# Optimization experiments

Measured on AMD Instinct MI355X. Metric: run time of the kernel, lower is better.

Reference implementation:

```python
import jax, jax.numpy as jnp
import numpy as np
from jax import lax

STRIDES = (8, 16, 32, 64, 128)
LEVEL_HW = ((100, 128), (50, 64), (25, 32), (13, 16), (7, 8))
NUM_CLASSES = 80
PRE_NMS_THRESH = 0.05
PRE_NMS_TOPK = 1000
NMS_THRESH = 0.6
MAX_DET = 100
CLS_OFFSET = 1.0e4  # > max image coordinate, separates classes for joint NMS


def setup_inputs() -> dict:
    key = jax.random.key(0)
    B = 16
    ks = jax.random.split(key, 3 * len(LEVEL_HW))
    inp = {}
    i = 0
    for lvl, (h, w) in enumerate(LEVEL_HW):
        # shift logits down so sigmoid scores are mostly below the 0.05 candidate
        # threshold (realistic detection sparsity)
        inp[f"logits_p{lvl + 3}"] = jax.random.normal(ks[i], (B, NUM_CLASSES, h, w), jnp.float32) - 4.0; i += 1
        inp[f"bbox_p{lvl + 3}"] = jax.random.uniform(ks[i], (B, 4, h, w), jnp.float32, minval=0.0, maxval=64.0); i += 1
        inp[f"ctr_p{lvl + 3}"] = jax.random.normal(ks[i], (B, 1, h, w), jnp.float32); i += 1
    inp["im_info"] = jnp.tile(jnp.array([[800.0, 1024.0]], jnp.float32), (B, 1))
    return inp


def _locations(h, w, stride):
    # FCOSLocation: center of each stride cell -> [HW, 2] as (x, y)
    sx = jnp.arange(w, dtype=jnp.float32) * stride + stride // 2
    sy = jnp.arange(h, dtype=jnp.float32) * stride + stride // 2
    yy, xx = jnp.meshgrid(sy, sx, indexing="ij")
    return jnp.stack([xx.reshape(-1), yy.reshape(-1)], axis=-1)


def _nms_single(boxes, scores, classes):
    # boxes [K,4], scores [K] (descending), classes [K] int
    off = classes.astype(jnp.float32)[:, None] * CLS_OFFSET
    nb = boxes + off  # class-offset trick -> per-class NMS in one pass
    areas = jnp.maximum(nb[:, 2] - nb[:, 0], 0.0) * jnp.maximum(nb[:, 3] - nb[:, 1], 0.0)

    def body(sc, _):
        i = jnp.argmax(sc)
        s = sc[i]
        bi = nb[i]
        xx1 = jnp.maximum(bi[0], nb[:, 0])
        yy1 = jnp.maximum(bi[1], nb[:, 1])
        xx2 = jnp.minimum(bi[2], nb[:, 2])
        yy2 = jnp.minimum(bi[3], nb[:, 3])
        inter = jnp.maximum(xx2 - xx1, 0.0) * jnp.maximum(yy2 - yy1, 0.0)
        iou = inter / (areas[i] + areas - inter + 1e-9)
        sc2 = jnp.where(iou >= NMS_THRESH, -jnp.inf, sc).at[i].set(-jnp.inf)
        return sc2, (i, s > 0.0)

    _, (idxs, valid) = lax.scan(body, scores, None, length=MAX_DET)
    det = jnp.concatenate(
        [boxes[idxs], scores[idxs][:, None], classes[idxs].astype(jnp.float32)[:, None]],
        axis=-1,
    )  # [MAX_DET, 6] = x1,y1,x2,y2,score,class
    return jnp.where(valid[:, None], det, 0.0)


def _forward(logits_p3, bbox_p3, ctr_p3, logits_p4, bbox_p4, ctr_p4,
             logits_p5, bbox_p5, ctr_p5, logits_p6, bbox_p6, ctr_p6,
             logits_p7, bbox_p7, ctr_p7, im_info):
    levels = [(logits_p3, bbox_p3, ctr_p3), (logits_p4, bbox_p4, ctr_p4),
              (logits_p5, bbox_p5, ctr_p5), (logits_p6, bbox_p6, ctr_p6),
              (logits_p7, bbox_p7, ctr_p7)]
    scores_l, boxes_l = [], []
    for (lg, rg, ct), stride in zip(levels, STRIDES):
        B, C, H, W = lg.shape
        cls = jax.nn.sigmoid(lg).transpose(0, 2, 3, 1).reshape(B, H * W, C)
        cen = jax.nn.sigmoid(ct).transpose(0, 2, 3, 1).reshape(B, H * W, 1)
        # candidate threshold on raw class prob, then modulate by centerness
        comb = jnp.where(cls > PRE_NMS_THRESH, cls * cen, 0.0)
        locs = _locations(H, W, stride)  # [HW, 2]
        reg = rg.transpose(0, 2, 3, 1).reshape(B, H * W, 4)  # (l, t, r, b)
        bx = jnp.stack([locs[None, :, 0] - reg[..., 0],
                        locs[None, :, 1] - reg[..., 1],
                        locs[None, :, 0] + reg[..., 2],
                        locs[None, :, 1] + reg[..., 3]], axis=-1)
        scores_l.append(comb)
        boxes_l.append(bx)
    scores = jnp.concatenate(scores_l, axis=1)  # [B, N, C]
    boxes = jnp.concatenate(boxes_l, axis=1)    # [B, N, 4]
    B, N, C = scores.shape
    vals, idx = lax.top_k(scores.reshape(B, N * C), PRE_NMS_TOPK)  # [B, K]
    loc = idx // C
    cls_id = idx % C
    cand = jnp.take_along_axis(boxes, loc[..., None], axis=1)  # [B, K, 4]
    h = im_info[:, 0:1]
    w = im_info[:, 1:2]
    x1 = jnp.clip(cand[..., 0], 0.0, w - 1.0)
    y1 = jnp.clip(cand[..., 1], 0.0, h - 1.0)
    x2 = jnp.clip(cand[..., 2], 0.0, w - 1.0)
    y2 = jnp.clip(cand[..., 3], 0.0, h - 1.0)
    cand = jnp.stack([x1, y1, x2, y2], axis=-1)
    sc = jnp.where(vals > 0.0, jnp.sqrt(jnp.maximum(vals, 0.0) + 1e-12), 0.0)
    return jax.vmap(_nms_single)(cand, sc, cls_id)  # [B, MAX_DET, 6]


def reference(logits_p3, bbox_p3, ctr_p3, logits_p4, bbox_p4, ctr_p4,
              logits_p5, bbox_p5, ctr_p5, logits_p6, bbox_p6, ctr_p6,
              logits_p7, bbox_p7, ctr_p7, im_info):
    return _forward(logits_p3, bbox_p3, ctr_p3, logits_p4, bbox_p4, ctr_p4,
                    logits_p5, bbox_p5, ctr_p5, logits_p6, bbox_p6, ctr_p6,
                    logits_p7, bbox_p7, ctr_p7, im_info)
```

## Files before the change

kernel.cpp:

```cpp
#include <hip/hip_runtime.h>
#include <math.h>

#pragma clang fp contract(off)

#define NB 16
#define NC 80
#define NTOT 17064
#define TOPK 1000
#define NBINS 8192
#define CAP 4096
#define MAXDET 100
#define NREP 2
#define CNTSTRIDE 64
#define CHUNK 128

struct Ptrs {
    const float* lg[5];
    const float* bb[5];
    const float* ct[5];
};

__device__ __forceinline__ void level_of(int n, int& l, int& hw, int& W,
                                         int& stride, int& half, int& HW) {
    if (n < 12800)      { l = 0; hw = n;         W = 128; stride = 8;   half = 4;  HW = 12800; }
    else if (n < 16000) { l = 1; hw = n - 12800; W = 64;  stride = 16;  half = 8;  HW = 3200;  }
    else if (n < 16800) { l = 2; hw = n - 16000; W = 32;  stride = 32;  half = 16; HW = 800;   }
    else if (n < 17008) { l = 3; hw = n - 16800; W = 16;  stride = 64;  half = 32; HW = 208;   }
    else                { l = 4; hw = n - 17008; W = 8;   stride = 128; half = 64; HW = 56;    }
}

__device__ __forceinline__ float fast_sig(float x) {
    float e = __expf(-x);
    return __builtin_amdgcn_rcpf(1.0f + e);
}

template<int HW4, int NF4>
__device__ __forceinline__ void hist_level(const float* lgb, const float* ctb,
                                           int tid, int bx, int gx, unsigned* lh) {
    for (int i0 = bx * 256; i0 < NF4; i0 += gx * 256) {
        int i = i0 + tid;
        if (i < NF4) {
            int c   = i / HW4;
            int hwf = i - c * HW4;
            float4 v  = *(const float4*)(lgb + c * (HW4 * 4) + hwf * 4);
            if (v.x > -2.95f || v.y > -2.95f || v.z > -2.95f || v.w > -2.95f) {
                float4 cv = *(const float4*)(ctb + hwf * 4);
                float xs[4] = {v.x, v.y, v.z, v.w};
                float cs[4] = {cv.x, cv.y, cv.z, cv.w};
#pragma unroll
                for (int j = 0; j < 4; ++j) {
                    float x = xs[j];
                    if (x > -2.95f) {
                        float cls = fast_sig(x);
                        if (cls > 0.04999f) {
                            bool in = true;
                            if (cls < 0.05001f) {
                                float ex = 1.0f / (1.0f + expf(-x));
                                in = ex > 0.05f;
                            }
                            if (in) {
                                float cen = fast_sig(cs[j]);
                                float comb = cls * cen;
                                unsigned bits = __float_as_uint(comb);
                                bits = (bits > 32u) ? bits - 32u : 0u;
                                atomicAdd(&lh[bits >> 19], 1u);
                            }
                        }
                    }
                }
            }
        }
    }
}

__global__ void __launch_bounds__(256) k_histA(Ptrs p, unsigned* hist) {
    __shared__ unsigned lh[NBINS];
    int b = blockIdx.y, tid = threadIdx.x, bx = blockIdx.x, gx = gridDim.x;
    for (int i = tid; i < NBINS; i += 256) lh[i] = 0;
    __syncthreads();

    hist_level<3200, 256000>(p.lg[0] + (size_t)b * NC * 12800, p.ct[0] + (size_t)b * 12800, tid, bx, gx, lh);
    hist_level< 800,  64000>(p.lg[1] + (size_t)b * NC * 3200,  p.ct[1] + (size_t)b * 3200,  tid, bx, gx, lh);
    hist_level< 200,  16000>(p.lg[2] + (size_t)b * NC * 800,   p.ct[2] + (size_t)b * 800,   tid, bx, gx, lh);
    hist_level<  52,   4160>(p.lg[3] + (size_t)b * NC * 208,   p.ct[3] + (size_t)b * 208,   tid, bx, gx, lh);
    hist_level<  14,   1120>(p.lg[4] + (size_t)b * NC * 56,    p.ct[4] + (size_t)b * 56,    tid, bx, gx, lh);

    __syncthreads();
    unsigned* h = hist + ((size_t)(bx & (NREP - 1)) * NB + b) * NBINS;
    for (int i = tid; i < NBINS; i += 256) {
        unsigned v = lh[i];
        if (v) atomicAdd(&h[i], v);
    }
}

__global__ void __launch_bounds__(256) k_thresh(const unsigned* hist, unsigned* T) {
    __shared__ unsigned hl[NBINS];
    __shared__ unsigned wtot[4];
    __shared__ int Tf;
    int b = blockIdx.x, tid = threadIdx.x, lane = tid & 63, wv = tid >> 6;
    if (tid == 0) Tf = 0;
    for (int i = tid; i < NBINS; i += 256) {
        unsigned s = 0;
        for (int r = 0; r < NREP; ++r)
            s += hist[((size_t)r * NB + b) * NBINS + i];
        hl[i] = s;
    }
    __syncthreads();
    int base = tid * 32;
    unsigned mysum = 0;
#pragma unroll
    for (int i = 0; i < 32; ++i) mysum += hl[base + i];
    unsigned incl = mysum;
#pragma unroll
    for (int off = 1; off < 64; off <<= 1) {
        unsigned v = __shfl_down(incl, off);
        if (lane + off < 64) incl += v;
    }
    if (lane == 0) wtot[wv] = incl;
    __syncthreads();
    unsigned above = 0;
    for (int w = wv + 1; w < 4; ++w) above += wtot[w];
    unsigned sufincl = incl + above;
    unsigned excl = sufincl - mysum;
    if (excl < TOPK && sufincl >= TOPK) {
        unsigned running = excl;
        for (int bin = base + 31; bin >= base; --bin) {
            running += hl[bin];
            if (running >= TOPK) { Tf = bin; break; }
        }
    }
    __syncthreads();
    if (tid == 0) T[b] = (unsigned)Tf;
}

template<int HW4, int NF4, int LVOFF>
__device__ __forceinline__ void compact_level(const float* lgb, const float* ctb,
        int tid, int lane, int bx, int gx, unsigned Tb, float xpre,
        unsigned* cntb, unsigned long long* selb, unsigned long long ltmask) {
    for (int i0 = bx * 256; i0 < NF4; i0 += gx * 256) {
        int i = i0 + tid;
        bool f0 = false, f1 = false, f2 = false, f3 = false;
        unsigned long long k0 = 0, k1 = 0, k2 = 0, k3 = 0;
        if (i < NF4) {
            int c   = i / HW4;
            int hwf = i - c * HW4;
            float4 v = *(const float4*)(lgb + c * (HW4 * 4) + hwf * 4);
            if (v.x > xpre || v.y > xpre || v.z > xpre || v.w > xpre) {
                float4 cv = *(const float4*)(ctb + hwf * 4);
                int nbase = LVOFF + hwf * 4;
#define DO_J(J, X, CT, F, K)                                                  \
                if ((X) > xpre) {                                             \
                    float cls = 1.0f / (1.0f + expf(-(X)));                   \
                    if (cls > 0.05f) {                                        \
                        float cen = 1.0f / (1.0f + expf(-(CT)));              \
                        float comb = cls * cen;                               \
                        unsigned bits = __float_as_uint(comb);                \
                        if ((bits >> 19) >= Tb) {                             \
                            unsigned idx = (unsigned)((nbase + (J)) * NC + c);\
                            K = ((unsigned long long)bits << 32) |            \
                                (0xFFFFFFFFu - idx);                          \
                            F = true;                                         \
                        }                                                     \
                    }                                                         \
                }
                DO_J(0, v.x, cv.x, f0, k0)
                DO_J(1, v.y, cv.y, f1, k1)
                DO_J(2, v.z, cv.z, f2, k2)
                DO_J(3, v.w, cv.w, f3, k3)
#undef DO_J
            }
        }
        unsigned long long m0 = __ballot(f0), m1 = __ballot(f1);
        unsigned long long m2 = __ballot(f2), m3 = __ballot(f3);
        if ((m0 | m1 | m2 | m3) == 0ULL) continue;
        unsigned t0 = (unsigned)__popcll(m0), t1 = (unsigned)__popcll(m1);
        unsigned t2 = (unsigned)__popcll(m2), t3 = (unsigned)__popcll(m3);
        unsigned total = t0 + t1 + t2 + t3;
        int basep = 0;
        if (lane == 0) basep = (int)atomicAdd(cntb, total);
        basep = __shfl(basep, 0);
        if (f0) { int pos = basep + (int)__popcll(m0 & ltmask);                       if (pos < CAP) selb[pos] = k0; }
        if (f1) { int pos = basep + (int)t0 + (int)__popcll(m1 & ltmask);             if (pos < CAP) selb[pos] = k1; }
        if (f2) { int pos = basep + (int)(t0 + t1) + (int)__popcll(m2 & ltmask);      if (pos < CAP) selb[pos] = k2; }
        if (f3) { int pos = basep + (int)(t0 + t1 + t2) + (int)__popcll(m3 & ltmask); if (pos < CAP) selb[pos] = k3; }
    }
}

__global__ void __launch_bounds__(256) k_compactB(Ptrs p, const unsigned* T,
                                                  unsigned* cnt2, unsigned long long* sel) {
    int b = blockIdx.y, tid = threadIdx.x, lane = tid & 63;
    int bx = blockIdx.x, gx = gridDim.x;
    unsigned Tb = T[b];
    float mthr = __uint_as_float(Tb << 19);
    float xpre = -2.95f;
    if (mthr > 1e-37f && mthr < 1.0f) {
        float lm = logf(mthr / (1.0f - mthr)) - 0.01f;
        if (lm > xpre) xpre = lm;
    }
    unsigned long long ltmask = (1ULL << lane) - 1ULL;
    unsigned* cntb = cnt2 + (size_t)b * CNTSTRIDE;
    unsigned long long* selb = sel + (size_t)b * CAP;
    compact_level<3200, 256000,     0>(p.lg[0] + (size_t)b * NC * 12800, p.ct[0] + (size_t)b * 12800, tid, lane, bx, gx, Tb, xpre, cntb, selb, ltmask);
    compact_level< 800,  64000, 12800>(p.lg[1] + (size_t)b * NC * 3200,  p.ct[1] + (size_t)b * 3200,  tid, lane, bx, gx, Tb, xpre, cntb, selb, ltmask);
    compact_level< 200,  16000, 16000>(p.lg[2] + (size_t)b * NC * 800,   p.ct[2] + (size_t)b * 800,   tid, lane, bx, gx, Tb, xpre, cntb, selb, ltmask);
    compact_level<  52,   4160, 16800>(p.lg[3] + (size_t)b * NC * 208,   p.ct[3] + (size_t)b * 208,   tid, lane, bx, gx, Tb, xpre, cntb, selb, ltmask);
    compact_level<  14,   1120, 17008>(p.lg[4] + (size_t)b * NC * 56,    p.ct[4] + (size_t)b * 56,    tid, lane, bx, gx, Tb, xpre, cntb, selb, ltmask);
}

__global__ void __launch_bounds__(256) k_rankdec(Ptrs p, const unsigned* cnt,
                                                 const unsigned long long* sel,
                                                 const float* im_info, float* cand) {
    __shared__ __align__(16) unsigned long long keys[CAP];
    int b = blockIdx.y, tid = threadIdx.x;
    unsigned M = cnt[(size_t)b * CNTSTRIDE];
    if (M > CAP) M = CAP;
    int s0 = blockIdx.x * 256;
    if (s0 >= (int)M) return;
    int Mpad = (int)((M + 1u) & ~1u);
    for (int i = tid; i < Mpad; i += 256)
        keys[i] = (i < (int)M) ? sel[(size_t)b * CAP + i] : 0ULL;
    __syncthreads();

    int s = s0 + tid;
    if (s >= (int)M) return;
    unsigned long long k = keys[s];
    int rank = 0;
    for (int j = 0; j < Mpad; j += 2) {
        ulonglong2 kk = *(const ulonglong2*)&keys[j];
        rank += (kk.x > k) ? 1 : 0;
        rank += (kk.y > k) ? 1 : 0;
    }
    if (rank >= TOPK) return;

    float Him = im_info[b * 2 + 0], Wim = im_info[b * 2 + 1];
    float xmax = Wim - 1.0f, ymax = Him - 1.0f;
    unsigned sb = (unsigned)(k >> 32);
    unsigned idx = 0xFFFFFFFFu - (unsigned)(k & 0xFFFFFFFFu);
    float val = __uint_as_float(sb);
    int n = idx / NC, c = idx - n * NC;
    int l, hw, W, stride, half, HW;
    level_of(n, l, hw, W, stride, half, HW);
    int wx = hw % W, hy = hw / W;
    float locx = (float)(wx * stride + half);
    float locy = (float)(hy * stride + half);
    const float* bb = p.bb[l] + (size_t)b * 4 * HW + hw;
    float r0 = bb[0], r1 = bb[(size_t)HW], r2 = bb[(size_t)2 * HW], r3 = bb[(size_t)3 * HW];
    float x1 = locx - r0, y1 = locy - r1, x2 = locx + r2, y2 = locy + r3;
    x1 = fminf(fmaxf(x1, 0.f), xmax);
    y1 = fminf(fmaxf(y1, 0.f), ymax);
    x2 = fminf(fmaxf(x2, 0.f), xmax);
    y2 = fminf(fmaxf(y2, 0.f), ymax);
    float scv = sqrtf(val + 1e-12f);
    float off = (float)c * 10000.0f;
    float a0 = x1 + off, a1 = y1 + off, a2 = x2 + off, a3 = y2 + off;
    float area = fmaxf(a2 - a0, 0.f) * fmaxf(a3 - a1, 0.f);
    float* dst = cand + ((size_t)b * TOPK + rank) * 12;
    *(float4*)(dst + 0) = make_float4(x1, y1, x2, y2);
    *(float4*)(dst + 4) = make_float4(a0, a1, a2, a3);
    *(float4*)(dst + 8) = make_float4(area, scv, (float)c, 0.f);
}

__global__ void __launch_bounds__(64) k_nms(const unsigned* cnt, const float* cand,
                                            float* out) {
    __shared__ float4 s_ob[CHUNK], s_nb[CHUNK], s_ms[CHUNK];
    int b = blockIdx.x, lane = threadIdx.x;
    unsigned M = cnt[(size_t)b * CNTSTRIDE];
    if (M > CAP) M = CAP;
    int ncand = (int)M < TOPK ? (int)M : TOPK;
    const float* src = cand + (size_t)b * TOPK * 12;
    float* ob = out + (size_t)b * MAXDET * 6;

    int na = 0;
    float4 a0b = make_float4(0.f, 0.f, 0.f, 0.f);
    float4 a1b = make_float4(0.f, 0.f, 0.f, 0.f);
    float a0a = 0.f, a1a = 0.f;

    for (int base = 0; base < ncand && na < MAXDET; base += CHUNK) {
        int cn = ncand - base; if (cn > CHUNK) cn = CHUNK;
        for (int cidx = lane; cidx < cn; cidx += 64) {
            const float* s = src + (size_t)(base + cidx) * 12;
            s_ob[cidx] = *(const float4*)(s + 0);
            s_nb[cidx] = *(const float4*)(s + 4);
            s_ms[cidx] = *(const float4*)(s + 8);
        }
        __syncthreads();
        for (int r = 0; r < cn && na < MAXDET; ++r) {
            float4 cb = s_nb[r];
            float ca = s_ms[r].x;
            bool sup = false;
            if (lane < na) {
                float xx1 = fmaxf(a0b.x, cb.x);
                float yy1 = fmaxf(a0b.y, cb.y);
                float xx2 = fminf(a0b.z, cb.z);
                float yy2 = fminf(a0b.w, cb.w);
                float inter = fmaxf(xx2 - xx1, 0.f) * fmaxf(yy2 - yy1, 0.f);
                float iou = inter / (((a0a + ca) - inter) + 1e-9f);
                sup = (iou >= 0.6f);
            }
            if (lane + 64 < na) {
                float xx1 = fmaxf(a1b.x, cb.x);
                float yy1 = fmaxf(a1b.y, cb.y);
                float xx2 = fminf(a1b.z, cb.z);
                float yy2 = fminf(a1b.w, cb.w);
                float inter = fmaxf(xx2 - xx1, 0.f) * fmaxf(yy2 - yy1, 0.f);
                float iou = inter / (((a1a + ca) - inter) + 1e-9f);
                sup |= (iou >= 0.6f);
            }
            if (__ballot(sup) == 0ULL) {
                if (lane == (na & 63)) {
                    if (na < 64) { a0b = cb; a0a = ca; }
                    else         { a1b = cb; a1a = ca; }
                }
                if (lane == 0) {
                    float4 o4 = s_ob[r]; float4 m4 = s_ms[r];
                    ob[na * 6 + 0] = o4.x; ob[na * 6 + 1] = o4.y;
                    ob[na * 6 + 2] = o4.z; ob[na * 6 + 3] = o4.w;
                    ob[na * 6 + 4] = m4.y; ob[na * 6 + 5] = m4.z;
                }
                ++na;
            }
        }
        __syncthreads();
    }
    for (int q = na * 6 + lane; q < MAXDET * 6; q += 64)
        ob[q] = 0.f;
}

extern "C" void kernel_launch(void* const* d_in, const int* in_sizes, int n_in,
                              void* d_out, int out_size, void* d_ws, size_t ws_size,
                              hipStream_t stream) {
    Ptrs p;
    for (int l = 0; l < 5; ++l) {
        p.lg[l] = (const float*)d_in[3 * l + 0];
        p.bb[l] = (const float*)d_in[3 * l + 1];
        p.ct[l] = (const float*)d_in[3 * l + 2];
    }
    const float* im_info = (const float*)d_in[15];
    float* out = (float*)d_out;

    unsigned char* w = (unsigned char*)d_ws;
    unsigned* hist          = (unsigned*)(w);
    unsigned* cnt2          = (unsigned*)(w + 1048576);
    unsigned* T             = (unsigned*)(w + 1052672);
    unsigned long long* sel = (unsigned long long*)(w + 1052928);
    float* cand             = (float*)(w + 1577216);

    hipMemsetAsync(w, 0, 1052928, stream);

    k_histA<<<dim3(64, NB), 256, 0, stream>>>(p, hist);
    k_thresh<<<NB, 256, 0, stream>>>(hist, T);
    k_compactB<<<dim3(128, NB), 256, 0, stream>>>(p, T, cnt2, sel);
    k_rankdec<<<dim3(16, NB), 256, 0, stream>>>(p, cnt2, sel, im_info, cand);
    k_nms<<<NB, 64, 0, stream>>>(cnt2, cand, out);
}
```

Before: 241.4 us.

## Replace full histogram with coarse 64-bin histogram above 0.08, drop memset

The histogram pass now counts only combined scores above a fixed 0.08 floor into 64 bins per wave in shared memory, writing per-block partials without global atomics or a large zeroed workspace. The threshold kernel reduces these partials and falls back to a full per-image 8192-bin histogram only when fewer than TOPK candidates lie above the floor. A tighter logit prefilter skips more sigmoid work, the memset is removed by zeroing counters inside the histogram kernel, and both histogram and compaction loops process two float4 loads per thread per iteration. The fallback path is single-block per image and slow if it triggers.

Result: no change. 238.8 us (-1.1%).

```diff
diff --git a/kernel.cpp b/kernel.cpp
--- a/kernel.cpp
+++ b/kernel.cpp
@@ -10,9 +10,9 @@
 #define NBINS 8192
 #define CAP 4096
 #define MAXDET 100
-#define NREP 2
 #define CNTSTRIDE 64
 #define CHUNK 128
+#define GH 128
 
 struct Ptrs {
     const float* lg[5];
@@ -34,15 +34,81 @@
     return __builtin_amdgcn_rcpf(1.0f + e);
 }
 
+#define HG_ELEM(X, CT)                                                        \
+    if ((X) > -2.47f) {                             \
+        float cls = fast_sig(X);                                              \
+        float cen = fast_sig(CT);                                             \
+        unsigned bits = __float_as_uint(cls * cen);                           \
+        if (bits >= FB_LO) {                                                  \
+            int lb = (int)((bits - 32u) >> 19) - BINBASE;                     \
+            lb = (lb < 0) ? 0 : ((lb > 63) ? 63 : lb);                        \
+            atomicAdd(&whv[lb], 1u);                                          \
+        }                                                                     \
+    }
+
 template<int HW4, int NF4>
-__device__ __forceinline__ void hist_level(const float* lgb, const float* ctb,
-                                           int tid, int bx, int gx, unsigned* lh) {
-    for (int i0 = bx * 256; i0 < NF4; i0 += gx * 256) {
+__device__ __forceinline__ void histg_level(const float* lgb, const float* ctb,
+        int tid, int bx, int gx, unsigned FB_LO, int BINBASE, unsigned* whv) {
+    for (int i0 = bx * 512; i0 < NF4; i0 += gx * 512) {
+        int ia = i0 + tid, ib = i0 + 256 + tid;
+        bool la = ia < NF4, lb2 = ib < NF4;
+        float4 va = make_float4(-9.f, -9.f, -9.f, -9.f);
+        float4 vb = make_float4(-9.f, -9.f, -9.f, -9.f);
+        int hwa = 0, hwb = 0;
+        if (la) {
+            int c = ia / HW4; hwa = ia - c * HW4;
+            va = *(const float4*)(lgb + c * (HW4 * 4) + hwa * 4);
+        }
+        if (lb2) {
+            int c = ib / HW4; hwb = ib - c * HW4;
+            vb = *(const float4*)(lgb + c * (HW4 * 4) + hwb * 4);
+        }
+        if (va.x > -2.47f || va.y > -2.47f || va.z > -2.47f || va.w > -2.47f) {
+            float4 cv = *(const float4*)(ctb + hwa * 4);
+            HG_ELEM(va.x, cv.x) HG_ELEM(va.y, cv.y)
+            HG_ELEM(va.z, cv.z) HG_ELEM(va.w, cv.w)
+        }
+        if (vb.x > -2.47f || vb.y > -2.47f || vb.z > -2.47f || vb.w > -2.47f) {
+            float4 cv = *(const float4*)(ctb + hwb * 4);
+            HG_ELEM(vb.x, cv.x) HG_ELEM(vb.y, cv.y)
+            HG_ELEM(vb.z, cv.z) HG_ELEM(vb.w, cv.w)
+        }
+    }
+}
+#undef HG_ELEM
+
+__global__ void __launch_bounds__(256) k_histB(Ptrs p, unsigned* hist, unsigned* cnt2) {
+    __shared__ unsigned wh[4][64];
+    int b = blockIdx.y, tid = threadIdx.x, bx = blockIdx.x, gx = gridDim.x;
+    int wv = tid >> 6;
+    if (bx == 0 && tid == 0) cnt2[(size_t)b * CNTSTRIDE] = 0;
+    ((unsigned*)wh)[tid] = 0;
+    __syncthreads();
+    unsigned FB_LO = __float_as_uint(0.08f) - 64u;
+    int BINBASE = (int)(__float_as_uint(0.08f) >> 19);
+    unsigned* whv = wh[wv];
+
+    histg_level<3200, 256000>(p.lg[0] + (size_t)b * NC * 12800, p.ct[0] + (size_t)b * 12800, tid, bx, gx, FB_LO, BINBASE, whv);
+    histg_level< 800,  64000>(p.lg[1] + (size_t)b * NC * 3200,  p.ct[1] + (size_t)b * 3200,  tid, bx, gx, FB_LO, BINBASE, whv);
+    histg_level< 200,  16000>(p.lg[2] + (size_t)b * NC * 800,   p.ct[2] + (size_t)b * 800,   tid, bx, gx, FB_LO, BINBASE, whv);
+    histg_level<  52,   4160>(p.lg[3] + (size_t)b * NC * 208,   p.ct[3] + (size_t)b * 208,   tid, bx, gx, FB_LO, BINBASE, whv);
+    histg_level<  14,   1120>(p.lg[4] + (size_t)b * NC * 56,    p.ct[4] + (size_t)b * 56,    tid, bx, gx, FB_LO, BINBASE, whv);
+
+    __syncthreads();
+    if (tid < 64) {
+        unsigned s = wh[0][tid] + wh[1][tid] + wh[2][tid] + wh[3][tid];
+        hist[((size_t)b * GH + bx) * 64 + tid] = s;
+    }
+}
+
+template<int HW4, int NF4>
+__device__ __forceinline__ void histf_level(const float* lgb, const float* ctb,
+                                            int tid, unsigned* hist) {
+    for (int i0 = 0; i0 < NF4; i0 += 256) {
         int i = i0 + tid;
         if (i < NF4) {
-            int c   = i / HW4;
-            int hwf = i - c * HW4;
-            float4 v  = *(const float4*)(lgb + c * (HW4 * 4) + hwf * 4);
+            int c = i / HW4, hwf = i - c * HW4;
+            float4 v = *(const float4*)(lgb + c * (HW4 * 4) + hwf * 4);
             if (v.x > -2.95f || v.y > -2.95f || v.z > -2.95f || v.w > -2.95f) {
                 float4 cv = *(const float4*)(ctb + hwf * 4);
                 float xs[4] = {v.x, v.y, v.z, v.w};
@@ -54,16 +120,13 @@
                         float cls = fast_sig(x);
                         if (cls > 0.04999f) {
                             bool in = true;
-                            if (cls < 0.05001f) {
-                                float ex = 1.0f / (1.0f + expf(-x));
-                                in = ex > 0.05f;
-                            }
+                            if (cls < 0.05001f)
+                                in = (1.0f / (1.0f + expf(-x))) > 0.05f;
                             if (in) {
                                 float cen = fast_sig(cs[j]);
-                                float comb = cls * cen;
-                                unsigned bits = __float_as_uint(comb);
-                                bits = (bits > 32u) ? bits - 32u : 0u;
-                                atomicAdd(&lh[bits >> 19], 1u);
+                                unsigned bits = __float_as_uint(cls * cen);
+                                unsigned cb = (bits > 32u) ? bits - 32u : 0u;
+                                atomicAdd(&hist[cb >> 19], 1u);
                             }
                         }
                     }
@@ -73,118 +136,144 @@
     }
 }
 
-__global__ void __launch_bounds__(256) k_histA(Ptrs p, unsigned* hist) {
-    __shared__ unsigned lh[NBINS];
-    int b = blockIdx.y, tid = threadIdx.x, bx = blockIdx.x, gx = gridDim.x;
-    for (int i = tid; i < NBINS; i += 256) lh[i] = 0;
-    __syncthreads();
-
-    hist_level<3200, 256000>(p.lg[0] + (size_t)b * NC * 12800, p.ct[0] + (size_t)b * 12800, tid, bx, gx, lh);
-    hist_level< 800,  64000>(p.lg[1] + (size_t)b * NC * 3200,  p.ct[1] + (size_t)b * 3200,  tid, bx, gx, lh);
-    hist_level< 200,  16000>(p.lg[2] + (size_t)b * NC * 800,   p.ct[2] + (size_t)b * 800,   tid, bx, gx, lh);
-    hist_level<  52,   4160>(p.lg[3] + (size_t)b * NC * 208,   p.ct[3] + (size_t)b * 208,   tid, bx, gx, lh);
-    hist_level<  14,   1120>(p.lg[4] + (size_t)b * NC * 56,    p.ct[4] + (size_t)b * 56,    tid, bx, gx, lh);
-
-    __syncthreads();
-    unsigned* h = hist + ((size_t)(bx & (NREP - 1)) * NB + b) * NBINS;
-    for (int i = tid; i < NBINS; i += 256) {
-        unsigned v = lh[i];
-        if (v) atomicAdd(&h[i], v);
-    }
-}
-
-__global__ void __launch_bounds__(256) k_thresh(const unsigned* hist, unsigned* T) {
-    __shared__ unsigned hl[NBINS];
-    __shared__ unsigned wtot[4];
-    __shared__ int Tf;
-    int b = blockIdx.x, tid = threadIdx.x, lane = tid & 63, wv = tid >> 6;
-    if (tid == 0) Tf = 0;
-    for (int i = tid; i < NBINS; i += 256) {
-        unsigned s = 0;
-        for (int r = 0; r < NREP; ++r)
-            s += hist[((size_t)r * NB + b) * NBINS + i];
-        hl[i] = s;
-    }
-    __syncthreads();
-    int base = tid * 32;
-    unsigned mysum = 0;
-#pragma unroll
-    for (int i = 0; i < 32; ++i) mysum += hl[base + i];
-    unsigned incl = mysum;
-#pragma unroll
-    for (int off = 1; off < 64; off <<= 1) {
-        unsigned v = __shfl_down(incl, off);
-        if (lane + off < 64) incl += v;
-    }
-    if (lane == 0) wtot[wv] = incl;
-    __syncthreads();
-    unsigned above = 0;
-    for (int w = wv + 1; w < 4; ++w) above += wtot[w];
-    unsigned sufincl = incl + above;
-    unsigned excl = sufincl - mysum;
-    if (excl < TOPK && sufincl >= TOPK) {
-        unsigned running = excl;
-        for (int bin = base + 31; bin >= base; --bin) {
-            running += hl[bin];
-            if (running >= TOPK) { Tf = bin; break; }
-        }
-    }
-    __syncthreads();
-    if (tid == 0) T[b] = (unsigned)Tf;
-}
+__global__ void __launch_bounds__(256) k_thresh(Ptrs p, const unsigned* hist,
+                                                unsigned* T) {
+    __shared__ unsigned part[4][64];
+    __shared__ unsigned red[64];
+    __shared__ unsigned fullh[NBINS];
+    __shared__ int s_T, s_ok;
+    int b = blockIdx.x, tid = threadIdx.x;
+    int bin = tid & 63, grp = tid >> 6;
+    int BINBASE = (int)(__float_as_uint(0.08f) >> 19);
+
+    unsigned s = 0;
+    for (int blk = grp; blk < GH; blk += 4)
+        s += hist[((size_t)b * GH + blk) * 64 + bin];
+    part[grp][bin] = s;
+    __syncthreads();
+    if (tid < 64) red[tid] = part[0][tid] + part[1][tid] + part[2][tid] + part[3][tid];
+    __syncthreads();
+    if (tid == 0) {
+        unsigned suf1 = 0;
+        for (int i = 1; i < 64; ++i) suf1 += red[i];
+        unsigned run = 0; int Tl = 0;
+        for (int i = 63; i >= 1; --i) {
+            run += red[i];
+            if (run >= TOPK) { Tl = i; break; }
+        }
+        s_ok = (suf1 >= TOPK);
+        s_T = Tl + BINBASE;
+    }
+    __syncthreads();
+
+    if (!s_ok) {
+        for (int i = tid; i < NBINS; i += 256) fullh[i] = 0;
+        __syncthreads();
+        histf_level<3200, 256000>(p.lg[0] + (size_t)b * NC * 12800, p.ct[0] + (size_t)b * 12800, tid, fullh);
+        histf_level< 800,  64000>(p.lg[1] + (size_t)b * NC * 3200,  p.ct[1] + (size_t)b * 3200,  tid, fullh);
+        histf_level< 200,  16000>(p.lg[2] + (size_t)b * NC * 800,   p.ct[2] + (size_t)b * 800,   tid, fullh);
+        histf_level<  52,   4160>(p.lg[3] + (size_t)b * NC * 208,   p.ct[3] + (size_t)b * 208,   tid, fullh);
+        histf_level<  14,   1120>(p.lg[4] + (size_t)b * NC * 56,    p.ct[4] + (size_t)b * 56,    tid, fullh);
+        __syncthreads();
+        if (tid == 0) {
+            unsigned run = 0; int Tf = 0;
+            for (int i = NBINS - 1; i >= 0; --i) {
+                run += fullh[i];
+                if (run >= TOPK) { Tf = i; break; }
+            }
+            s_T = Tf;
+        }
+        __syncthreads();
+    }
+    if (tid == 0) T[b] = (unsigned)s_T;
+}
+
+#define CD_J(J, X, CT, NB0, CC, F, K)                                         \
+    if ((X) > xpre) {                                                         \
+        float cls = 1.0f / (1.0f + expf(-(X)));                               \
+        if (cls > 0.05f) {                                                    \
+            float cen = 1.0f / (1.0f + expf(-(CT)));                          \
+            float comb = cls * cen;                                           \
+            unsigned bits = __float_as_uint(comb);                            \
+            if ((bits >> 19) >= Tb) {                                         \
+                unsigned idx = (unsigned)(((NB0) + (J)) * NC + (CC));         \
+                K = ((unsigned long long)bits << 32) | (0xFFFFFFFFu - idx);   \
+                F = true;                                                     \
+            }                                                                 \
+        }                                                                     \
+    }
 
 template<int HW4, int NF4, int LVOFF>
 __device__ __forceinline__ void compact_level(const float* lgb, const float* ctb,
         int tid, int lane, int bx, int gx, unsigned Tb, float xpre,
         unsigned* cntb, unsigned long long* selb, unsigned long long ltmask) {
-    for (int i0 = bx * 256; i0 < NF4; i0 += gx * 256) {
-        int i = i0 + tid;
-        bool f0 = false, f1 = false, f2 = false, f3 = false;
-        unsigned long long k0 = 0, k1 = 0, k2 = 0, k3 = 0;
-        if (i < NF4) {
-            int c   = i / HW4;
-            int hwf = i - c * HW4;
-            float4 v = *(const float4*)(lgb + c * (HW4 * 4) + hwf * 4);
-            if (v.x > xpre || v.y > xpre || v.z > xpre || v.w > xpre) {
-                float4 cv = *(const float4*)(ctb + hwf * 4);
-                int nbase = LVOFF + hwf * 4;
-#define DO_J(J, X, CT, F, K)                                                  \
-                if ((X) > xpre) {                                             \
-                    float cls = 1.0f / (1.0f + expf(-(X)));                   \
-                    if (cls > 0.05f) {                                        \
-                        float cen = 1.0f / (1.0f + expf(-(CT)));              \
-                        float comb = cls * cen;                               \
-                        unsigned bits = __float_as_uint(comb);                \
-                        if ((bits >> 19) >= Tb) {                             \
-                            unsigned idx = (unsigned)((nbase + (J)) * NC + c);\
-                            K = ((unsigned long long)bits << 32) |            \
-                                (0xFFFFFFFFu - idx);                          \
-                            F = true;                                         \
-                        }                                                     \
-                    }                                                         \
-                }
-                DO_J(0, v.x, cv.x, f0, k0)
-                DO_J(1, v.y, cv.y, f1, k1)
-                DO_J(2, v.z, cv.z, f2, k2)
-                DO_J(3, v.w, cv.w, f3, k3)
-#undef DO_J
-            }
-        }
-        unsigned long long m0 = __ballot(f0), m1 = __ballot(f1);
-        unsigned long long m2 = __ballot(f2), m3 = __ballot(f3);
-        if ((m0 | m1 | m2 | m3) == 0ULL) continue;
-        unsigned t0 = (unsigned)__popcll(m0), t1 = (unsigned)__popcll(m1);
-        unsigned t2 = (unsigned)__popcll(m2), t3 = (unsigned)__popcll(m3);
-        unsigned total = t0 + t1 + t2 + t3;
-        int basep = 0;
-        if (lane == 0) basep = (int)atomicAdd(cntb, total);
-        basep = __shfl(basep, 0);
-        if (f0) { int pos = basep + (int)__popcll(m0 & ltmask);                       if (pos < CAP) selb[pos] = k0; }
-        if (f1) { int pos = basep + (int)t0 + (int)__popcll(m1 & ltmask);             if (pos < CAP) selb[pos] = k1; }
-        if (f2) { int pos = basep + (int)(t0 + t1) + (int)__popcll(m2 & ltmask);      if (pos < CAP) selb[pos] = k2; }
-        if (f3) { int pos = basep + (int)(t0 + t1 + t2) + (int)__popcll(m3 & ltmask); if (pos < CAP) selb[pos] = k3; }
-    }
-}
+    for (int i0 = bx * 512; i0 < NF4; i0 += gx * 512) {
+        int ia = i0 + tid, ib2 = i0 + 256 + tid;
+        bool la = ia < NF4, lb2 = ib2 < NF4;
+        float4 va = make_float4(-9.f, -9.f, -9.f, -9.f);
+        float4 vb = make_float4(-9.f, -9.f, -9.f, -9.f);
+        int hwa = 0, hwb = 0, cca = 0, ccb = 0;
+        if (la) {
+            cca = ia / HW4; hwa = ia - cca * HW4;
+            va = *(const float4*)(lgb + cca * (HW4 * 4) + hwa * 4);
+        }
+        if (lb2) {
+            ccb = ib2 / HW4; hwb = ib2 - ccb * HW4;
+            vb = *(const float4*)(lgb + ccb * (HW4 * 4) + hwb * 4);
+        }
+        {
+            bool f0 = false, f1 = false, f2 = false, f3 = false;
+            unsigned long long k0 = 0, k1 = 0, k2 = 0, k3 = 0;
+            if (va.x > xpre || va.y > xpre || va.z > xpre || va.w > xpre) {
+                float4 cv = *(const float4*)(ctb + hwa * 4);
+                int nb0 = LVOFF + hwa * 4;
+                CD_J(0, va.x, cv.x, nb0, cca, f0, k0)
+                CD_J(1, va.y, cv.y, nb0, cca, f1, k1)
+                CD_J(2, va.z, cv.z, nb0, cca, f2, k2)
+                CD_J(3, va.w, cv.w, nb0, cca, f3, k3)
+            }
+            unsigned long long m0 = __ballot(f0), m1 = __ballot(f1);
+            unsigned long long m2 = __ballot(f2), m3 = __ballot(f3);
+            if (m0 | m1 | m2 | m3) {
+                unsigned t0 = (unsigned)__popcll(m0), t1 = (unsigned)__popcll(m1);
+                unsigned t2 = (unsigned)__popcll(m2), t3 = (unsigned)__popcll(m3);
+                int basep = 0;
+                if (lane == 0) basep = (int)atomicAdd(cntb, t0 + t1 + t2 + t3);
+                basep = __shfl(basep, 0);
+                if (f0) { int pos = basep + (int)__popcll(m0 & ltmask);                       if (pos < CAP) selb[pos] = k0; }
+                if (f1) { int pos = basep + (int)t0 + (int)__popcll(m1 & ltmask);             if (pos < CAP) selb[pos] = k1; }
+                if (f2) { int pos = basep + (int)(t0 + t1) + (int)__popcll(m2 & ltmask);      if (pos < CAP) selb[pos] = k2; }
+                if (f3) { int pos = basep + (int)(t0 + t1 + t2) + (int)__popcll(m3 & ltmask); if (pos < CAP) selb[pos] = k3; }
+            }
+        }
+        {
+            bool f0 = false, f1 = false, f2 = false, f3 = false;
+            unsigned long long k0 = 0, k1 = 0, k2 = 0, k3 = 0;
+            if (vb.x > xpre || vb.y > xpre || vb.z > xpre || vb.w > xpre) {
+                float4 cv = *(const float4*)(ctb + hwb * 4);
+                int nb0 = LVOFF + hwb * 4;
+                CD_J(0, vb.x, cv.x, nb0, ccb, f0, k0)
+                CD_J(1, vb.y, cv.y, nb0, ccb, f1, k1)
+                CD_J(2, vb.z, cv.z, nb0, ccb, f2, k2)
+                CD_J(3, vb.w, cv.w, nb0, ccb, f3, k3)
+            }
+            unsigned long long m0 = __ballot(f0), m1 = __ballot(f1);
+            unsigned long long m2 = __ballot(f2), m3 = __ballot(f3);
+            if (m0 | m1 | m2 | m3) {
+                unsigned t0 = (unsigned)__popcll(m0), t1 = (unsigned)__popcll(m1);
+                unsigned t2 = (unsigned)__popcll(m2), t3 = (unsigned)__popcll(m3);
+                int basep = 0;
+                if (lane == 0) basep = (int)atomicAdd(cntb, t0 + t1 + t2 + t3);
+                basep = __shfl(basep, 0);
+                if (f0) { int pos = basep + (int)__popcll(m0 & ltmask);                       if (pos < CAP) selb[pos] = k0; }
+                if (f1) { int pos = basep + (int)t0 + (int)__popcll(m1 & ltmask);             if (pos < CAP) selb[pos] = k1; }
+                if (f2) { int pos = basep + (int)(t0 + t1) + (int)__popcll(m2 & ltmask);      if (pos < CAP) selb[pos] = k2; }
+                if (f3) { int pos = basep + (int)(t0 + t1 + t2) + (int)__popcll(m3 & ltmask); if (pos < CAP) selb[pos] = k3; }
+            }
+        }
+    }
+}
+#undef CD_J
 
 __global__ void __launch_bounds__(256) k_compactB(Ptrs p, const unsigned* T,
                                                   unsigned* cnt2, unsigned long long* sel) {
@@ -337,19 +426,17 @@
     }
     const float* im_info = (const float*)d_in[15];
     float* out = (float*)d_out;
-
     unsigned char* w = (unsigned char*)d_ws;
+
     unsigned* hist          = (unsigned*)(w);
-    unsigned* cnt2          = (unsigned*)(w + 1048576);
-    unsigned* T             = (unsigned*)(w + 1052672);
-    unsigned long long* sel = (unsigned long long*)(w + 1052928);
-    float* cand             = (float*)(w + 1577216);
-
-    hipMemsetAsync(w, 0, 1052928, stream);
-
-    k_histA<<<dim3(64, NB), 256, 0, stream>>>(p, hist);
-    k_thresh<<<NB, 256, 0, stream>>>(hist, T);
-    k_compactB<<<dim3(128, NB), 256, 0, stream>>>(p, T, cnt2, sel);
+    unsigned* cnt2          = (unsigned*)(w + 524288);
+    unsigned* T             = (unsigned*)(w + 528384);
+    unsigned long long* sel = (unsigned long long*)(w + 528640);
+    float* cand             = (float*)(w + 1052928);
+
+    k_histB<<<dim3(GH, NB), 256, 0, stream>>>(p, hist, cnt2);
+    k_thresh<<<NB, 256, 0, stream>>>(p, hist, T);
+    k_compactB<<<dim3(GH, NB), 256, 0, stream>>>(p, T, cnt2, sel);
     k_rankdec<<<dim3(16, NB), 256, 0, stream>>>(p, cnt2, sel, im_info, cand);
     k_nms<<<NB, 64, 0, stream>>>(cnt2, cand, out);
 }
```
